# Kernel optimization log

Measured on AMD Instinct MI355X. Metric: run time of the kernel, lower is better.

## Reference

```python
import jax, jax.numpy as jnp
import numpy as np

WS = 8
NUM_HEADS = 4
DIM = 64
H = W = 128
B = 16
EPS = 1e-5


def _rel_pos_index(ws):
    coords = np.stack(np.meshgrid(np.arange(ws), np.arange(ws), indexing='ij'))  # (2,ws,ws)
    cf = coords.reshape(2, -1)
    rel = (cf[:, :, None] - cf[:, None, :]).transpose(1, 2, 0).astype(np.int64)
    rel[..., 0] += ws - 1
    rel[..., 1] += ws - 1
    rel[..., 0] *= 2 * ws - 1
    return jnp.asarray(rel.sum(-1))  # (ws*ws, ws*ws)

_RPI = _rel_pos_index(WS)


def _ln_hw(x, g, b):
    # LayerNorm over last two dims (H,W) of (B,C,H,W), affine shape (H,W)
    mu = x.mean(axis=(-2, -1), keepdims=True)
    var = ((x - mu) ** 2).mean(axis=(-2, -1), keepdims=True)
    return (x - mu) / jnp.sqrt(var + EPS) * g + b


def _ln_c(x, g, b):
    mu = x.mean(-1, keepdims=True)
    var = ((x - mu) ** 2).mean(-1, keepdims=True)
    return (x - mu) / jnp.sqrt(var + EPS) * g + b


def _win_part(x, ws):
    # (B,C,H,W) -> (B*nW, ws*ws, C)
    b, c, hh, ww = x.shape
    x = x.reshape(b, c, hh // ws, ws, ww // ws, ws)
    return x.transpose(0, 2, 4, 3, 5, 1).reshape(b * (hh // ws) * (ww // ws), ws * ws, c)


def _win_rev(w, ws, hh, ww, b):
    # (B*nW, ws*ws, C) -> (B,C,H,W)
    c = w.shape[-1]
    w = w.reshape(b, hh // ws, ww // ws, ws, ws, c)
    return w.transpose(0, 5, 1, 3, 2, 4).reshape(b, c, hh, ww)


def _forward(x, lclg1_ln1_g, lclg1_ln1_b, lclg1_conv_w, lclg1_conv_b, lclg1_ln2_g, lclg1_ln2_b,
             lclg2_ln1_g, lclg2_ln1_b, lclg2_conv_w, lclg2_conv_b, lclg2_ln2_g, lclg2_ln2_b,
             pos1, pos2, q_w, q_b, kv_w, kv_b, rpb_table, gamma, proj_w, proj_b,
             norm2_g, norm2_b, fc1_w, fc1_b, fc2_w, fc2_b):
    b, c, hh, ww = x.shape
    h = NUM_HEADS
    hd = c // h
    n = WS * WS
    scale = hd ** -0.5

    def lclg(z, g1, b1, cw, cb, g2, b2):
        z = _ln_hw(z, g1, b1)
        z = jnp.einsum('oc,bchw->bohw', cw, z) + cb[None, :, None, None]  # 1x1 conv
        return jax.nn.gelu(_ln_hw(z, g2, b2), approximate=False)

    x1 = lclg(x, lclg1_ln1_g, lclg1_ln1_b, lclg1_conv_w, lclg1_conv_b, lclg1_ln2_g, lclg1_ln2_b)
    x2 = lclg(x, lclg2_ln1_g, lclg2_ln1_b, lclg2_conv_w, lclg2_conv_b, lclg2_ln2_g, lclg2_ln2_b)

    x1w = _win_part(x1, WS) + pos1  # (B_, N, C)
    x2w = _win_part(x2, WS) + pos2
    bw = x1w.shape[0]

    q = (x1w @ q_w.T + q_b).reshape(bw, n, h, hd).transpose(0, 2, 1, 3) * scale  # (B_,h,N,hd)
    kv = (x2w @ kv_w.T + kv_b).reshape(bw, n, 2, h, hd).transpose(2, 0, 3, 1, 4)
    k, v = kv[0], kv[1]

    attn = jnp.einsum('bhnd,bhmd->bhnm', q, k)
    bias = rpb_table[_RPI.reshape(-1)].reshape(n, n, h).transpose(2, 0, 1)  # (h,N,N)
    attn = jax.nn.softmax(attn + bias[None], axis=-1)
    o = jnp.einsum('bhnm,bhmd->bhnd', attn, v)  # (B_,h,N,hd)

    # LAM_Module: attention over head_dim channels of (B_,h,N,hd)
    y = o.transpose(0, 3, 1, 2).reshape(bw, hd, h * n)  # (B_,hd,h*N)
    energy = jnp.einsum('bik,bjk->bij', y, y)  # (B_,hd,hd)
    lam = jnp.einsum('bij,bjk->bik', jax.nn.softmax(energy, axis=-1), y)
    y = (gamma * lam + y).reshape(bw, hd, h, n).transpose(0, 2, 3, 1)  # (B_,h,N,hd)

    xo = y.transpose(0, 2, 1, 3).reshape(bw, n, c) + q.transpose(0, 2, 1, 3).reshape(bw, n, c) + x1w
    xo = xo @ proj_w.T + proj_b

    xo = _win_rev(xo, WS, hh, ww, b)  # (B,C,H,W)

    # MLP with pre-norm residual over channel dim
    t = xo.reshape(b, c, hh * ww).transpose(0, 2, 1)  # (B,HW,C)
    tn = _ln_c(t, norm2_g, norm2_b)
    t = t + (jax.nn.gelu(tn @ fc1_w.T + fc1_b, approximate=False) @ fc2_w.T + fc2_b)
    return t.transpose(0, 2, 1).reshape(b, c, hh, ww)


def setup_inputs() -> dict:
    key = jax.random.key(0)
    ks = jax.random.split(key, 16)
    d = DIM

    def rn(i, shape, sc=0.02):
        return jax.random.normal(ks[i], shape, jnp.float32) * sc

    return dict(
        x=jax.random.normal(ks[0], (B, d, H, W), jnp.float32),
        lclg1_ln1_g=jnp.ones((H, W), jnp.float32), lclg1_ln1_b=jnp.zeros((H, W), jnp.float32),
        lclg1_conv_w=rn(1, (d, d)), lclg1_conv_b=jnp.zeros((d,), jnp.float32),
        lclg1_ln2_g=jnp.ones((H, W), jnp.float32), lclg1_ln2_b=jnp.zeros((H, W), jnp.float32),
        lclg2_ln1_g=jnp.ones((H, W), jnp.float32), lclg2_ln1_b=jnp.zeros((H, W), jnp.float32),
        lclg2_conv_w=rn(2, (d, d)), lclg2_conv_b=jnp.zeros((d,), jnp.float32),
        lclg2_ln2_g=jnp.ones((H, W), jnp.float32), lclg2_ln2_b=jnp.zeros((H, W), jnp.float32),
        pos1=jnp.ones((1, WS * WS, d), jnp.float32),
        pos2=jnp.ones((1, WS * WS, d), jnp.float32),
        q_w=rn(3, (d, d)), q_b=jnp.zeros((d,), jnp.float32),
        kv_w=rn(4, (2 * d, d)), kv_b=jnp.zeros((2 * d,), jnp.float32),
        rpb_table=rn(5, ((2 * WS - 1) ** 2, NUM_HEADS)),
        gamma=jnp.full((1,), 0.1, jnp.float32),
        proj_w=rn(6, (d, d)), proj_b=jnp.zeros((d,), jnp.float32),
        norm2_g=jnp.ones((d,), jnp.float32), norm2_b=jnp.zeros((d,), jnp.float32),
        fc1_w=rn(7, (d, d)), fc1_b=jnp.zeros((d,), jnp.float32),
        fc2_w=rn(8, (d, d)), fc2_b=jnp.zeros((d,), jnp.float32),
    )


def reference(x, lclg1_ln1_g, lclg1_ln1_b, lclg1_conv_w, lclg1_conv_b, lclg1_ln2_g, lclg1_ln2_b,
              lclg2_ln1_g, lclg2_ln1_b, lclg2_conv_w, lclg2_conv_b, lclg2_ln2_g, lclg2_ln2_b,
              pos1, pos2, q_w, q_b, kv_w, kv_b, rpb_table, gamma, proj_w, proj_b,
              norm2_g, norm2_b, fc1_w, fc1_b, fc2_w, fc2_b):
    return _forward(x, lclg1_ln1_g, lclg1_ln1_b, lclg1_conv_w, lclg1_conv_b, lclg1_ln2_g, lclg1_ln2_b,
                    lclg2_ln1_g, lclg2_ln1_b, lclg2_conv_w, lclg2_conv_b, lclg2_ln2_g, lclg2_ln2_b,
                    pos1, pos2, q_w, q_b, kv_w, kv_b, rpb_table, gamma, proj_w, proj_b,
                    norm2_g, norm2_b, fc1_w, fc1_b, fc2_w, fc2_b)
```

## Files before the change

### kernel.cpp

```cpp
#include <hip/hip_runtime.h>
#include <hip/hip_bf16.h>

typedef __hip_bfloat16 bf16;
typedef __attribute__((ext_vector_type(8))) short short8;
typedef __attribute__((ext_vector_type(4))) short short4v;
typedef __attribute__((ext_vector_type(4))) float float4v;
typedef __attribute__((ext_vector_type(2))) float float2v;

__device__ __forceinline__ short f2bs(float f){
    union { bf16 h; short s; } u; u.h = __float2bfloat16(f); return u.s;
}
__device__ __forceinline__ float bs2f(short s){
    return __uint_as_float(((unsigned)(unsigned short)s) << 16);
}
__device__ __forceinline__ float gelu_exact(float x){
    return 0.5f * x * (1.0f + erff(x * 0.70710678118654752440f));
}
#define MFMA(a,b,c) __builtin_amdgcn_mfma_f32_16x16x32_bf16((a),(b),(c),0,0,0)

#define HW 16384
#define NPLANE 1048576
#define EPS 1e-5f
#define LS 72

#define OFF_W1   0
#define OFF_W2   4096
#define OFF_QW   8192
#define OFF_KVW  12288
#define OFF_PW   20480
#define OFF_FW1  24576
#define OFF_FW2  28672

__global__ __launch_bounds__(256) void k_pre(const float* __restrict__ x,
                                             float* __restrict__ mu,
                                             float* __restrict__ rinv,
                                             const float* __restrict__ w1, const float* __restrict__ w2,
                                             const float* __restrict__ qw, const float* __restrict__ kvw,
                                             const float* __restrict__ pw, const float* __restrict__ fw1,
                                             const float* __restrict__ fw2,
                                             short* __restrict__ wb, float* __restrict__ rowsum){
    int bi = blockIdx.x;
    int tid = threadIdx.x;
    if (bi < 1024){
        const float* p = x + (size_t)bi * HW;
        float s = 0.f, ss = 0.f;
        for (int i = tid; i < HW/4; i += 256){
            float4v v = *(const float4v*)(p + i*4);
            #pragma unroll
            for (int k = 0; k < 4; k++){ s += v[k]; ss += v[k]*v[k]; }
        }
        __shared__ float rs[256], rss[256];
        rs[tid] = s; rss[tid] = ss; __syncthreads();
        for (int st = 128; st > 0; st >>= 1){
            if (tid < st){ rs[tid] += rs[tid+st]; rss[tid] += rss[tid+st]; }
            __syncthreads();
        }
        if (tid == 0){
            float m = rs[0] * (1.f/HW);
            float v = rss[0] * (1.f/HW) - m*m;
            mu[bi] = m; rinv[bi] = rsqrtf(v + EPS);
        }
    } else if (bi < 1032){
        int wi = bi - 1024;
        const float* src = wi==0?w1: wi==1?w2: wi==2?qw: wi==3?kvw: wi==4?(kvw+4096): wi==5?pw: wi==6?fw1: fw2;
        short* dst = wb + wi*4096;
        int base = tid*16;
        short8 o8[2];
        #pragma unroll
        for (int k = 0; k < 2; k++){
            float4v v0 = *(const float4v*)(src + base + 8*k);
            float4v v1 = *(const float4v*)(src + base + 8*k + 4);
            #pragma unroll
            for (int j = 0; j < 4; j++){ o8[k][j] = f2bs(v0[j]); o8[k][4+j] = f2bs(v1[j]); }
        }
        *(short8*)&dst[base]     = o8[0];
        *(short8*)&dst[base + 8] = o8[1];
    } else {
        if (tid < 128){
            int br = tid >> 6, o = tid & 63;
            const float* W = br ? w2 : w1;
            float s = 0.f;
            for (int c = 0; c < 64; c++) s += W[o*64 + c];
            rowsum[br*64 + o] = s;
        }
    }
}

__global__ __launch_bounds__(256) void k_conv(const float* __restrict__ x,
                                              const float* __restrict__ mu,
                                              const float* __restrict__ rinv,
                                              const float* __restrict__ g1a, const float* __restrict__ b1a,
                                              const float* __restrict__ cb1,
                                              const float* __restrict__ g1b, const float* __restrict__ b1b,
                                              const float* __restrict__ cb2,
                                              const short* __restrict__ wb,
                                              const float* __restrict__ rowsum,
                                              float* __restrict__ partS, float* __restrict__ partQ){
    int blk = blockIdx.x;
    int b = blk >> 8; int tile = blk & 255; int hw0 = tile * 64;
    __shared__ __align__(16) short xn_bf[64*LS];
    const int tid = threadIdx.x;
    const int wq = tid >> 6, lane = tid & 63, qd = lane >> 4, col = lane & 15;
    const float4v zf = {0.f,0.f,0.f,0.f};

    {
        int p = tid & 63, cq = tid >> 6;
        const float* xb = x + (size_t)(b*64 + 16*cq)*HW + hw0 + p;
        float4v m4[4], r4[4];
        #pragma unroll
        for (int k = 0; k < 4; k++){
            m4[k] = *(const float4v*)(mu   + b*64 + 16*cq + 4*k);
            r4[k] = *(const float4v*)(rinv + b*64 + 16*cq + 4*k);
        }
        short8 o8[2];
        #pragma unroll
        for (int k = 0; k < 2; k++)
            #pragma unroll
            for (int j = 0; j < 8; j++){
                int jj = 8*k + j;
                float v = xb[(size_t)jj*HW];
                o8[k][j] = f2bs((v - m4[jj>>2][jj&3]) * r4[jj>>2][jj&3]);
            }
        *(short8*)&xn_bf[p*LS + 16*cq]     = o8[0];
        *(short8*)&xn_bf[p*LS + 16*cq + 8] = o8[1];
    }
    __syncthreads();

    #pragma unroll
    for (int br = 0; br < 2; br++){
        const short* W  = wb + (br ? OFF_W2 : OFF_W1);
        const float* cb = br ? cb2 : cb1;
        const float* gp = br ? g1b : g1a;
        const float* bp = br ? b1b : b1a;
        short8 a0 = *(const short8*)&W[(16*wq + col)*64 + 8*qd];
        short8 a1 = *(const short8*)&W[(16*wq + col)*64 + 32 + 8*qd];
        float cbv[4], rsv[4];
        #pragma unroll
        for (int r = 0; r < 4; r++){
            int o = 16*wq + 4*qd + r;
            cbv[r] = cb[o]; rsv[r] = rowsum[br*64 + o];
        }
        float sa[4]  = {0.f,0.f,0.f,0.f};
        float ssa[4] = {0.f,0.f,0.f,0.f};
        #pragma unroll
        for (int jn = 0; jn < 4; jn++){
            short8 bx0 = *(const short8*)&xn_bf[(16*jn + col)*LS + 8*qd];
            short8 bx1 = *(const short8*)&xn_bf[(16*jn + col)*LS + 32 + 8*qd];
            float4v acc = zf;
            acc = MFMA(a0, bx0, acc);
            acc = MFMA(a1, bx1, acc);
            int hw = hw0 + 16*jn + col;
            float gl = gp[hw], bl = bp[hw];
            #pragma unroll
            for (int r = 0; r < 4; r++){
                float v = gl*acc[r] + bl*rsv[r] + cbv[r];
                sa[r]  += v;
                ssa[r] += v*v;
            }
        }
        #pragma unroll
        for (int r = 0; r < 4; r++){
            float s = sa[r], ss = ssa[r];
            s += __shfl_xor(s, 1); ss += __shfl_xor(ss, 1);
            s += __shfl_xor(s, 2); ss += __shfl_xor(ss, 2);
            s += __shfl_xor(s, 4); ss += __shfl_xor(ss, 4);
            s += __shfl_xor(s, 8); ss += __shfl_xor(ss, 8);
            if (col == 0){
                int o = 16*wq + 4*qd + r;
                size_t pi = ((size_t)(br*16 + b)*64 + o)*256 + tile;
                partS[pi] = s; partQ[pi] = ss;
            }
        }
    }
}

__global__ __launch_bounds__(256) void k_fin(const float* __restrict__ partS,
                                             const float* __restrict__ partQ,
                                             float* __restrict__ mu2,
                                             float* __restrict__ rinv2){
    int row = blockIdx.x*4 + (threadIdx.x >> 6);
    int lane = threadIdx.x & 63;
    float4v a = *(const float4v*)(partS + (size_t)row*256 + lane*4);
    float4v b = *(const float4v*)(partQ + (size_t)row*256 + lane*4);
    float s  = a[0]+a[1]+a[2]+a[3];
    float ss = b[0]+b[1]+b[2]+b[3];
    #pragma unroll
    for (int st = 1; st < 64; st <<= 1){
        s  += __shfl_xor(s,  st);
        ss += __shfl_xor(ss, st);
    }
    if (lane == 0){
        float m = s * (1.f/HW);
        float v = ss * (1.f/HW) - m*m;
        mu2[row] = m; rinv2[row] = rsqrtf(v + EPS);
    }
}

__global__ __launch_bounds__(256, 4) void k_attn(const float* __restrict__ x, float* __restrict__ outp,
                                              const float* __restrict__ mu1, const float* __restrict__ rinv1,
                                              const float* __restrict__ rowsum,
                                              const float* __restrict__ cb1, const float* __restrict__ cb2,
                                              const float* __restrict__ g1a, const float* __restrict__ b1a,
                                              const float* __restrict__ g1b, const float* __restrict__ b1b,
                                              const float* __restrict__ mu2, const float* __restrict__ rinv2,
                                              const float* __restrict__ g2a, const float* __restrict__ b2a,
                                              const float* __restrict__ g2b, const float* __restrict__ b2b,
                                              const float* __restrict__ pos1, const float* __restrict__ pos2,
                                              const short* __restrict__ wb,
                                              const float* __restrict__ qb, const float* __restrict__ kvb,
                                              const float* __restrict__ rpb, const float* __restrict__ gammap,
                                              const float* __restrict__ pb,
                                              const float* __restrict__ n2g, const float* __restrict__ n2b,
                                              const float* __restrict__ fb1,
                                              const float* __restrict__ fb2){
    int B = blockIdx.x;
    int hy = (B & 7) | ((B >> 5) & 8);
    int wx = (((B >> 9) & 7) << 1) | ((B >> 3) & 1);
    int b  = (B >> 4) & 15;

    const short* qwb  = wb + OFF_QW;
    const short* kvwb = wb + OFF_KVW;
    const short* pwb  = wb + OFF_PW;
    const short* f1b  = wb + OFF_FW1;
    const short* f2b  = wb + OFF_FW2;

    __shared__ __align__(16) char smem[40464];
    short* bufA = (short*)smem;
    short* bufK = (short*)(smem + 9216);
    short* bufV = (short*)(smem + 18432);
    short* bufQ = (short*)(smem + 27648);
    float* rpb_lds = (float*)(smem + 36864);
    float* energyS = (float*)(smem + 36864);
    short* soft_bf = (short*)(smem + 37888);
    float* XOf  = (float*)(smem + 18432);
    short* tnb  = (short*)smem;
    short* h1b  = (short*)(smem + 9216);
    float* sumS = (float*)(smem + 36864);
    float* sqS  = (float*)(smem + 37888);
    float* muS  = (float*)(smem + 38912);
    float* rinvS= (float*)(smem + 39168);

    const int tid = threadIdx.x;
    const int wq = tid >> 6, lane = tid & 63, qd = lane >> 4, col = lane & 15;
    size_t base = (size_t)b * NPLANE;
    #define HWOF(t) ((hy*8 + ((t)>>3))*128 + wx*8 + ((t)&7))

    const float4v zf = {0.f,0.f,0.f,0.f};
    const short8 zero8 = {0,0,0,0,0,0,0,0};

    for (int i = tid; i < 900; i += 256) rpb_lds[i] = rpb[i];

    {
        int t = tid & 63, cq = tid >> 6;
        int hw = HWOF(t);
        const float* mup = mu1   + b*64 + 16*cq;
        const float* rvp = rinv1 + b*64 + 16*cq;
        float4v m4[4], r4[4];
        #pragma unroll
        for (int k = 0; k < 4; k++){
            m4[k] = *(const float4v*)(mup + 4*k);
            r4[k] = *(const float4v*)(rvp + 4*k);
        }
        short8 o8[2];
        #pragma unroll
        for (int k = 0; k < 2; k++)
            #pragma unroll
            for (int j = 0; j < 8; j++){
                int jj = 8*k + j;
                float v = x[base + (size_t)(16*cq + jj)*HW + hw];
                o8[k][j] = f2bs((v - m4[jj>>2][jj&3]) * r4[jj>>2][jj&3]);
            }
        *(short8*)&bufV[t*LS + 16*cq]     = o8[0];
        *(short8*)&bufV[t*LS + 16*cq + 8] = o8[1];
    }
    __syncthreads();

    {
        short8 a10 = *(const short8*)&wb[OFF_W1 + (16*wq + col)*64 + 8*qd];
        short8 a11 = *(const short8*)&wb[OFF_W1 + (16*wq + col)*64 + 32 + 8*qd];
        short8 a20 = *(const short8*)&wb[OFF_W2 + (16*wq + col)*64 + 8*qd];
        short8 a21 = *(const short8*)&wb[OFF_W2 + (16*wq + col)*64 + 32 + 8*qd];
        float cb1v[4], rs1v[4], m2a[4], rv2a[4];
        float cb2v[4], rs2v[4], m2b[4], rv2b[4];
        #pragma unroll
        for (int r = 0; r < 4; r++){
            int o = 16*wq + 4*qd + r;
            cb1v[r] = cb1[o]; rs1v[r] = rowsum[o];
            m2a[r] = mu2[b*64 + o]; rv2a[r] = rinv2[b*64 + o];
            cb2v[r] = cb2[o]; rs2v[r] = rowsum[64 + o];
            m2b[r] = mu2[1024 + b*64 + o]; rv2b[r] = rinv2[1024 + b*64 + o];
        }
        #pragma unroll
        for (int jn = 0; jn < 4; jn++){
            int t = 16*jn + col; int hw = HWOF(t);
            short8 bx0 = *(const short8*)&bufV[t*LS + 8*qd];
            short8 bx1 = *(const short8*)&bufV[t*LS + 32 + 8*qd];
            {
                float4v acc = zf;
                acc = MFMA(a10, bx0, acc);
                acc = MFMA(a11, bx1, acc);
                float gl = g1a[hw], bl = b1a[hw], gg = g2a[hw], bo = b2a[hw];
                float4v p4 = *(const float4v*)(pos1 + t*64 + 16*wq + 4*qd);
                short4v pk;
                #pragma unroll
                for (int r = 0; r < 4; r++){
                    float v = gl*acc[r] + bl*rs1v[r] + cb1v[r];
                    float z = (v - m2a[r]) * rv2a[r] * gg + bo;
                    pk[r] = f2bs(gelu_exact(z) + p4[r]);
                }
                *(short4v*)&bufA[t*LS + 16*wq + 4*qd] = pk;
            }
            {
                float4v acc = zf;
                acc = MFMA(a20, bx0, acc);
                acc = MFMA(a21, bx1, acc);
                float gl = g1b[hw], bl = b1b[hw], gg = g2b[hw], bo = b2b[hw];
                float4v p4 = *(const float4v*)(pos2 + t*64 + 16*wq + 4*qd);
                short4v pk;
                #pragma unroll
                for (int r = 0; r < 4; r++){
                    float v = gl*acc[r] + bl*rs2v[r] + cb2v[r];
                    float z = (v - m2b[r]) * rv2b[r] * gg + bo;
                    pk[r] = f2bs(gelu_exact(z) + p4[r]);
                }
                *(short4v*)&bufQ[t*LS + 16*wq + 4*qd] = pk;
            }
        }
    }
    __syncthreads();

    {
        short8 ax0 = *(const short8*)&bufQ[(16*wq + col)*LS + 8*qd];
        short8 ax1 = *(const short8*)&bufQ[(16*wq + col)*LS + 32 + 8*qd];
        #pragma unroll
        for (int jn = 0; jn < 4; jn++){
            int c = 16*jn + col;
            short8 wv0 = *(const short8*)&kvwb[(64 + c)*64 + 8*qd];
            short8 wv1 = *(const short8*)&kvwb[(64 + c)*64 + 32 + 8*qd];
            float4v acc = zf;
            acc = MFMA(ax0, wv0, acc);
            acc = MFMA(ax1, wv1, acc);
            float bv = kvb[64 + c];
            short4v pk;
            #pragma unroll
            for (int r = 0; r < 4; r++) pk[r] = f2bs(acc[r] + bv);
            *(short4v*)&bufV[c*LS + 16*wq + 4*qd] = pk;
        }
        short8 a0 = *(const short8*)&kvwb[(16*wq + col)*64 + 8*qd];
        short8 a1 = *(const short8*)&kvwb[(16*wq + col)*64 + 32 + 8*qd];
        float kbr[4];
        #pragma unroll
        for (int r = 0; r < 4; r++) kbr[r] = kvb[16*wq + 4*qd + r];
        #pragma unroll
        for (int jn = 0; jn < 4; jn++){
            int t = 16*jn + col;
            short8 bx0 = *(const short8*)&bufQ[t*LS + 8*qd];
            short8 bx1 = *(const short8*)&bufQ[t*LS + 32 + 8*qd];
            float4v acc = zf;
            acc = MFMA(a0, bx0, acc);
            acc = MFMA(a1, bx1, acc);
            short4v pk;
            #pragma unroll
            for (int r = 0; r < 4; r++) pk[r] = f2bs(acc[r] + kbr[r]);
            *(short4v*)&bufK[t*LS + 16*wq + 4*qd] = pk;
        }
    }
    __syncthreads();

    {
        short8 a0 = *(const short8*)&qwb[(16*wq + col)*64 + 8*qd];
        short8 a1 = *(const short8*)&qwb[(16*wq + col)*64 + 32 + 8*qd];
        float qbr[4];
        #pragma unroll
        for (int r = 0; r < 4; r++) qbr[r] = qb[16*wq + 4*qd + r];
        #pragma unroll
        for (int jn = 0; jn < 4; jn++){
            int t = 16*jn + col;
            short8 bx0 = *(const short8*)&bufA[t*LS + 8*qd];
            short8 bx1 = *(const short8*)&bufA[t*LS + 32 + 8*qd];
            float4v acc = zf;
            acc = MFMA(a0, bx0, acc);
            acc = MFMA(a1, bx1, acc);
            short4v pk;
            #pragma unroll
            for (int r = 0; r < 4; r++) pk[r] = f2bs((acc[r] + qbr[r]) * 0.25f);
            *(short4v*)&bufQ[t*LS + 16*wq + 4*qd] = pk;
        }
    }
    short4v xreg[4];
    #pragma unroll
    for (int h = 0; h < 4; h++){
        short4v xr;
        #pragma unroll
        for (int r = 0; r < 4; r++)
            xr[r] = bufA[(16*wq + 4*qd + r)*LS + 16*h + col];
        xreg[h] = xr;
    }
    __syncthreads();

    int idx_t[4][4];
    {
        int t = 16*wq + col, ty = t >> 3, tx = t & 7;
        #pragma unroll
        for (int jn = 0; jn < 4; jn++)
            #pragma unroll
            for (int r = 0; r < 4; r++){
                int u = 16*jn + 4*qd + r;
                idx_t[jn][r] = (ty - (u>>3) + 7)*15 + (tx - (u&7) + 7);
            }
    }

    for (int h = 0; h < 4; h++){
        short8 bq = *(const short8*)&bufQ[(16*wq + col)*LS + h*16 + (qd & 1)*8];
        float pr[4][4];
        #pragma unroll
        for (int jn = 0; jn < 4; jn++){
            short8 ak = *(const short8*)&bufK[(16*jn + col)*LS + h*16 + (qd & 1)*8];
            if (qd >= 2) ak = zero8;
            float4v acc = MFMA(ak, bq, zf);
            #pragma unroll
            for (int r = 0; r < 4; r++)
                pr[jn][r] = acc[r] + rpb_lds[idx_t[jn][r]*4 + h];
        }
        float m = pr[0][0];
        #pragma unroll
        for (int jn = 0; jn < 4; jn++)
            #pragma unroll
            for (int r = 0; r < 4; r++) m = fmaxf(m, pr[jn][r]);
        m = fmaxf(m, __shfl_xor(m, 16));
        m = fmaxf(m, __shfl_xor(m, 32));
        float s = 0.f;
        #pragma unroll
        for (int jn = 0; jn < 4; jn++)
            #pragma unroll
            for (int r = 0; r < 4; r++){ pr[jn][r] = __expf(pr[jn][r] - m); s += pr[jn][r]; }
        s += __shfl_xor(s, 16);
        s += __shfl_xor(s, 32);
        float rc = 1.f / s;
        #pragma unroll
        for (int jn = 0; jn < 4; jn++){
            short4v pk;
            #pragma unroll
            for (int r = 0; r < 4; r++) pk[r] = f2bs(pr[jn][r] * rc);
            *(short4v*)&bufA[(16*wq + col)*LS + 16*jn + 4*qd] = pk;
        }
        short8 ap0 = *(const short8*)&bufA[(16*wq + col)*LS + 8*qd];
        short8 ap1 = *(const short8*)&bufA[(16*wq + col)*LS + 32 + 8*qd];
        short8 bv0 = *(const short8*)&bufV[(h*16 + col)*LS + 8*qd];
        short8 bv1 = *(const short8*)&bufV[(h*16 + col)*LS + 32 + 8*qd];
        float4v acc_o = zf;
        acc_o = MFMA(ap0, bv0, acc_o);
        acc_o = MFMA(ap1, bv1, acc_o);
        __syncthreads();
        short4v ot;
        #pragma unroll
        for (int r = 0; r < 4; r++) ot[r] = f2bs(acc_o[r]);
        *(short4v*)&bufV[(h*16 + col)*LS + 16*wq + 4*qd] = ot;
        #pragma unroll
        for (int r = 0; r < 4; r++)
            bufK[(16*wq + 4*qd + r)*LS + h*16 + col] = ot[r];
    }
    __syncthreads();

    {
        float4v acc_e = zf;
        #pragma unroll
        for (int h = 0; h < 4; h++){
            short8 f0 = *(const short8*)&bufV[(h*16 + col)*LS + 8*qd];
            short8 f1 = *(const short8*)&bufV[(h*16 + col)*LS + 32 + 8*qd];
            acc_e = MFMA(f0, f0, acc_e);
            acc_e = MFMA(f1, f1, acc_e);
        }
        if (wq == 0){
            #pragma unroll
            for (int r = 0; r < 4; r++) energyS[(4*qd + r)*16 + col] = acc_e[r];
        }
    }
    __syncthreads();
    if (tid < 16){
        int i = tid; float m = -1e30f;
        for (int j = 0; j < 16; j++) m = fmaxf(m, energyS[i*16 + j]);
        float s = 0.f; float e[16];
        for (int j = 0; j < 16; j++){ e[j] = __expf(energyS[i*16 + j] - m); s += e[j]; }
        float rc = 1.f / s;
        for (int j = 0; j < 16; j++) soft_bf[i*32 + j] = f2bs(e[j] * rc);
        for (int j = 0; j < 16; j++) soft_bf[i*32 + 16 + j] = 0;
    }
    __syncthreads();

    {
        float gam = gammap[0];
        short8 asf = *(const short8*)&soft_bf[col*32 + 8*qd];
        #pragma unroll
        for (int h = 0; h < 4; h++){
            short8 ay = *(const short8*)&bufK[(16*wq + col)*LS + 16*h + (qd & 1)*8];
            float4v acc = MFMA(ay, asf, zf);
            short4v xv = xreg[h];
            #pragma unroll
            for (int r = 0; r < 4; r++){
                int ro = (16*wq + 4*qd + r)*LS + 16*h + col;
                float ot = bs2f(bufK[ro]);
                float qv = bs2f(bufQ[ro]);
                float xo = gam*acc[r] + ot + qv + bs2f(xv[r]);
                bufK[ro] = f2bs(xo);
            }
        }
    }
    __syncthreads();

    {
        short8 a0 = *(const short8*)&pwb[(16*wq + col)*64 + 8*qd];
        short8 a1 = *(const short8*)&pwb[(16*wq + col)*64 + 32 + 8*qd];
        float pbr[4];
        #pragma unroll
        for (int r = 0; r < 4; r++) pbr[r] = pb[16*wq + 4*qd + r];
        #pragma unroll
        for (int jn = 0; jn < 4; jn++){
            int t = 16*jn + col;
            short8 bx0 = *(const short8*)&bufK[t*LS + 8*qd];
            short8 bx1 = *(const short8*)&bufK[t*LS + 32 + 8*qd];
            float4v acc = zf;
            acc = MFMA(a0, bx0, acc);
            acc = MFMA(a1, bx1, acc);
            float2v w0 = {acc[0]+pbr[0], acc[1]+pbr[1]};
            float2v w1 = {acc[2]+pbr[2], acc[3]+pbr[3]};
            *(float2v*)&XOf[t*66 + 16*wq + 4*qd]     = w0;
            *(float2v*)&XOf[t*66 + 16*wq + 4*qd + 2] = w1;
        }
    }
    __syncthreads();

    {
        int p = tid & 63, qg = tid >> 6;
        float s = 0.f, ss = 0.f;
        #pragma unroll
        for (int j = 0; j < 8; j++){
            float2v v = *(const float2v*)&XOf[p*66 + qg*16 + 2*j];
            s += v[0]+v[1]; ss += v[0]*v[0] + v[1]*v[1];
        }
        sumS[qg*64 + p] = s; sqS[qg*64 + p] = ss;
    }
    __syncthreads();
    if (tid < 64){
        float s  = sumS[tid] + sumS[64+tid] + sumS[128+tid] + sumS[192+tid];
        float ss = sqS[tid]  + sqS[64+tid]  + sqS[128+tid]  + sqS[192+tid];
        float m = s * (1.f/64.f);
        float var = ss * (1.f/64.f) - m*m;
        muS[tid] = m; rinvS[tid] = rsqrtf(var + EPS);
    }
    __syncthreads();
    {
        int p = tid & 63, qg = tid >> 6;
        float m = muS[p], rv = rinvS[p];
        short8 o8[2];
        #pragma unroll
        for (int k = 0; k < 2; k++)
            #pragma unroll
            for (int j = 0; j < 8; j++){
                int c = qg*16 + k*8 + j;
                o8[k][j] = f2bs((XOf[p*66 + c] - m) * rv * n2g[c] + n2b[c]);
            }
        *(short8*)&tnb[p*LS + qg*16]     = o8[0];
        *(short8*)&tnb[p*LS + qg*16 + 8] = o8[1];
    }
    __syncthreads();
    {
        short8 a0 = *(const short8*)&f1b[(16*wq + col)*64 + 8*qd];
        short8 a1 = *(const short8*)&f1b[(16*wq + col)*64 + 32 + 8*qd];
        float fbr[4];
        #pragma unroll
        for (int r = 0; r < 4; r++) fbr[r] = fb1[16*wq + 4*qd + r];
        #pragma unroll
        for (int jn = 0; jn < 4; jn++){
            int t = 16*jn + col;
            short8 bx0 = *(const short8*)&tnb[t*LS + 8*qd];
            short8 bx1 = *(const short8*)&tnb[t*LS + 32 + 8*qd];
            float4v acc = zf;
            acc = MFMA(a0, bx0, acc);
            acc = MFMA(a1, bx1, acc);
            short4v pk;
            #pragma unroll
            for (int r = 0; r < 4; r++) pk[r] = f2bs(gelu_exact(acc[r] + fbr[r]));
            *(short4v*)&h1b[t*LS + 16*wq + 4*qd] = pk;
        }
    }
    __syncthreads();
    {
        short8 a0 = *(const short8*)&h1b[(16*wq + col)*LS + 8*qd];
        short8 a1 = *(const short8*)&h1b[(16*wq + col)*LS + 32 + 8*qd];
        #pragma unroll
        for (int jn = 0; jn < 4; jn++){
            int c2 = 16*jn + col;
            short8 f0 = *(const short8*)&f2b[c2*64 + 8*qd];
            short8 f1 = *(const short8*)&f2b[c2*64 + 32 + 8*qd];
            float4v acc = zf;
            acc = MFMA(a0, f0, acc);
            acc = MFMA(a1, f1, acc);
            float bv = fb2[c2];
            float4v ov;
            #pragma unroll
            for (int r = 0; r < 4; r++)
                ov[r] = acc[r] + bv + XOf[(16*wq + 4*qd + r)*66 + c2];
            int t0 = 16*wq + 4*qd;
            *(float4v*)(outp + base + (size_t)c2*HW + HWOF(t0)) = ov;
        }
    }
    #undef HWOF
}

extern "C" void kernel_launch(void* const* d_in, const int* in_sizes, int n_in,
                              void* d_out, int out_size, void* d_ws, size_t ws_size,
                              hipStream_t stream){
    const float* x        = (const float*)d_in[0];
    const float* l1_g1    = (const float*)d_in[1];
    const float* l1_b1    = (const float*)d_in[2];
    const float* l1_cw    = (const float*)d_in[3];
    const float* l1_cb    = (const float*)d_in[4];
    const float* l1_g2    = (const float*)d_in[5];
    const float* l1_b2    = (const float*)d_in[6];
    const float* l2_g1    = (const float*)d_in[7];
    const float* l2_b1    = (const float*)d_in[8];
    const float* l2_cw    = (const float*)d_in[9];
    const float* l2_cb    = (const float*)d_in[10];
    const float* l2_g2    = (const float*)d_in[11];
    const float* l2_b2    = (const float*)d_in[12];
    const float* pos1     = (const float*)d_in[13];
    const float* pos2     = (const float*)d_in[14];
    const float* q_w      = (const float*)d_in[15];
    const float* q_b      = (const float*)d_in[16];
    const float* kv_w     = (const float*)d_in[17];
    const float* kv_b     = (const float*)d_in[18];
    const float* rpb      = (const float*)d_in[19];
    const float* gamma    = (const float*)d_in[20];
    const float* proj_w   = (const float*)d_in[21];
    const float* proj_b   = (const float*)d_in[22];
    const float* norm2_g  = (const float*)d_in[23];
    const float* norm2_b  = (const float*)d_in[24];
    const float* fc1_w    = (const float*)d_in[25];
    const float* fc1_b    = (const float*)d_in[26];
    const float* fc2_w    = (const float*)d_in[27];
    const float* fc2_b    = (const float*)d_in[28];

    float* out = (float*)d_out;

    float* partS = (float*)d_ws;
    float* partQ = partS + (size_t)2048*256;
    float* mu1   = partQ + (size_t)2048*256;
    float* rinv1 = mu1 + 1024;
    float* mu2   = rinv1 + 1024;
    float* rinv2 = mu2 + 2048;
    float* rowsumG = rinv2 + 2048;
    short* wbuf  = (short*)(rowsumG + 128);

    k_pre  <<<1033, 256, 0, stream>>>(x, mu1, rinv1,
                                      l1_cw, l2_cw, q_w, kv_w, proj_w, fc1_w, fc2_w,
                                      wbuf, rowsumG);
    k_conv <<<4096, 256, 0, stream>>>(x, mu1, rinv1,
                                      l1_g1, l1_b1, l1_cb,
                                      l2_g1, l2_b1, l2_cb,
                                      wbuf, rowsumG,
                                      partS, partQ);
    k_fin  <<<512, 256, 0, stream>>>(partS, partQ, mu2, rinv2);
    k_attn <<<4096, 256, 0, stream>>>(x, out, mu1, rinv1, rowsumG,
                                      l1_cb, l2_cb,
                                      l1_g1, l1_b1, l2_g1, l2_b1,
                                      mu2, rinv2,
                                      l1_g2, l1_b2, l2_g2, l2_b2,
                                      pos1, pos2, wbuf, q_b, kv_b,
                                      rpb, gamma, proj_b,
                                      norm2_g, norm2_b, fc1_b, fc2_b);
}
```

Before: 322.9 us.

## Give conv-stat blocks four tiles each, hoist weights, and approximate erf in GELU

k_conv now has each block loop over four 64-pixel tiles, with weights, biases and row sums loaded once into registers, and both branches computed per tile. This cuts the grid from 4096 to 1024 blocks and shrinks the partial-sum buffers, so k_fin reduces 64 partials per row instead of 256. GELU swaps erff for an Abramowitz-Stegun polynomial using a fast reciprocal and __expf. That polynomial has error around 1e-7 and may shift accuracy slightly. The fewer, longer blocks also add per-tile barriers and may hide latency less well.

Result: faster. 316.5 us (-2.0%).

```diff
diff --git a/kernel.cpp b/kernel.cpp
--- a/kernel.cpp
+++ b/kernel.cpp
@@ -14,7 +14,14 @@
     return __uint_as_float(((unsigned)(unsigned short)s) << 16);
 }
 __device__ __forceinline__ float gelu_exact(float x){
-    return 0.5f * x * (1.0f + erff(x * 0.70710678118654752440f));
+    float ax = fabsf(x) * 0.70710678118654752440f;
+    float t  = __builtin_amdgcn_rcpf(fmaf(0.3275911f, ax, 1.0f));
+    float poly = t*fmaf(t, fmaf(t, fmaf(t, fmaf(t, 1.061405429f, -1.453152027f),
+                                 1.421413741f), -0.284496736f), 0.254829592f);
+    float e = __expf(-ax*ax);
+    float erfp = fmaf(-poly, e, 1.0f);
+    float er = copysignf(erfp, x);
+    return 0.5f * x * (1.0f + er);
 }
 #define MFMA(a,b,c) __builtin_amdgcn_mfma_f32_16x16x32_bf16((a),(b),(c),0,0,0)
 
@@ -86,7 +93,7 @@
     }
 }
 
-__global__ __launch_bounds__(256) void k_conv(const float* __restrict__ x,
+__global__ __launch_bounds__(256, 4) void k_conv(const float* __restrict__ x,
                                               const float* __restrict__ mu,
                                               const float* __restrict__ rinv,
                                               const float* __restrict__ g1a, const float* __restrict__ b1a,
@@ -97,81 +104,96 @@
                                               const float* __restrict__ rowsum,
                                               float* __restrict__ partS, float* __restrict__ partQ){
     int blk = blockIdx.x;
-    int b = blk >> 8; int tile = blk & 255; int hw0 = tile * 64;
+    int b = blk >> 6; int chunk = blk & 63;
     __shared__ __align__(16) short xn_bf[64*LS];
     const int tid = threadIdx.x;
     const int wq = tid >> 6, lane = tid & 63, qd = lane >> 4, col = lane & 15;
     const float4v zf = {0.f,0.f,0.f,0.f};
-
-    {
-        int p = tid & 63, cq = tid >> 6;
-        const float* xb = x + (size_t)(b*64 + 16*cq)*HW + hw0 + p;
-        float4v m4[4], r4[4];
-        #pragma unroll
-        for (int k = 0; k < 4; k++){
-            m4[k] = *(const float4v*)(mu   + b*64 + 16*cq + 4*k);
-            r4[k] = *(const float4v*)(rinv + b*64 + 16*cq + 4*k);
-        }
-        short8 o8[2];
-        #pragma unroll
-        for (int k = 0; k < 2; k++)
-            #pragma unroll
-            for (int j = 0; j < 8; j++){
-                int jj = 8*k + j;
-                float v = xb[(size_t)jj*HW];
-                o8[k][j] = f2bs((v - m4[jj>>2][jj&3]) * r4[jj>>2][jj&3]);
-            }
-        *(short8*)&xn_bf[p*LS + 16*cq]     = o8[0];
-        *(short8*)&xn_bf[p*LS + 16*cq + 8] = o8[1];
-    }
-    __syncthreads();
-
+    const int p = tid & 63, cq = tid >> 6;
+
+    float4v m4[4], r4[4];
     #pragma unroll
-    for (int br = 0; br < 2; br++){
-        const short* W  = wb + (br ? OFF_W2 : OFF_W1);
-        const float* cb = br ? cb2 : cb1;
-        const float* gp = br ? g1b : g1a;
-        const float* bp = br ? b1b : b1a;
-        short8 a0 = *(const short8*)&W[(16*wq + col)*64 + 8*qd];
-        short8 a1 = *(const short8*)&W[(16*wq + col)*64 + 32 + 8*qd];
-        float cbv[4], rsv[4];
-        #pragma unroll
-        for (int r = 0; r < 4; r++){
-            int o = 16*wq + 4*qd + r;
-            cbv[r] = cb[o]; rsv[r] = rowsum[br*64 + o];
-        }
-        float sa[4]  = {0.f,0.f,0.f,0.f};
-        float ssa[4] = {0.f,0.f,0.f,0.f};
+    for (int k = 0; k < 4; k++){
+        m4[k] = *(const float4v*)(mu   + b*64 + 16*cq + 4*k);
+        r4[k] = *(const float4v*)(rinv + b*64 + 16*cq + 4*k);
+    }
+    short8 a10 = *(const short8*)&wb[OFF_W1 + (16*wq + col)*64 + 8*qd];
+    short8 a11 = *(const short8*)&wb[OFF_W1 + (16*wq + col)*64 + 32 + 8*qd];
+    short8 a20 = *(const short8*)&wb[OFF_W2 + (16*wq + col)*64 + 8*qd];
+    short8 a21 = *(const short8*)&wb[OFF_W2 + (16*wq + col)*64 + 32 + 8*qd];
+    float cb1v[4], rs1v[4], cb2v[4], rs2v[4];
+    #pragma unroll
+    for (int r = 0; r < 4; r++){
+        int o = 16*wq + 4*qd + r;
+        cb1v[r] = cb1[o]; rs1v[r] = rowsum[o];
+        cb2v[r] = cb2[o]; rs2v[r] = rowsum[64 + o];
+    }
+    float sa[2][4]  = {{0.f,0.f,0.f,0.f},{0.f,0.f,0.f,0.f}};
+    float ssa[2][4] = {{0.f,0.f,0.f,0.f},{0.f,0.f,0.f,0.f}};
+
+    for (int tl = 0; tl < 4; tl++){
+        int hw0 = chunk*256 + tl*64;
+        {
+            const float* xb = x + (size_t)(b*64 + 16*cq)*HW + hw0 + p;
+            short8 o8[2];
+            #pragma unroll
+            for (int k = 0; k < 2; k++)
+                #pragma unroll
+                for (int j = 0; j < 8; j++){
+                    int jj = 8*k + j;
+                    float v = xb[(size_t)jj*HW];
+                    o8[k][j] = f2bs((v - m4[jj>>2][jj&3]) * r4[jj>>2][jj&3]);
+                }
+            *(short8*)&xn_bf[p*LS + 16*cq]     = o8[0];
+            *(short8*)&xn_bf[p*LS + 16*cq + 8] = o8[1];
+        }
+        __syncthreads();
         #pragma unroll
         for (int jn = 0; jn < 4; jn++){
             short8 bx0 = *(const short8*)&xn_bf[(16*jn + col)*LS + 8*qd];
             short8 bx1 = *(const short8*)&xn_bf[(16*jn + col)*LS + 32 + 8*qd];
-            float4v acc = zf;
-            acc = MFMA(a0, bx0, acc);
-            acc = MFMA(a1, bx1, acc);
             int hw = hw0 + 16*jn + col;
-            float gl = gp[hw], bl = bp[hw];
-            #pragma unroll
-            for (int r = 0; r < 4; r++){
-                float v = gl*acc[r] + bl*rsv[r] + cbv[r];
-                sa[r]  += v;
-                ssa[r] += v*v;
-            }
-        }
+            {
+                float4v acc = zf;
+                acc = MFMA(a10, bx0, acc);
+                acc = MFMA(a11, bx1, acc);
+                float gl = g1a[hw], bl = b1a[hw];
+                #pragma unroll
+                for (int r = 0; r < 4; r++){
+                    float v = gl*acc[r] + bl*rs1v[r] + cb1v[r];
+                    sa[0][r] += v; ssa[0][r] += v*v;
+                }
+            }
+            {
+                float4v acc = zf;
+                acc = MFMA(a20, bx0, acc);
+                acc = MFMA(a21, bx1, acc);
+                float gl = g1b[hw], bl = b1b[hw];
+                #pragma unroll
+                for (int r = 0; r < 4; r++){
+                    float v = gl*acc[r] + bl*rs2v[r] + cb2v[r];
+                    sa[1][r] += v; ssa[1][r] += v*v;
+                }
+            }
+        }
+        __syncthreads();
+    }
+
+    #pragma unroll
+    for (int br = 0; br < 2; br++)
         #pragma unroll
         for (int r = 0; r < 4; r++){
-            float s = sa[r], ss = ssa[r];
+            float s = sa[br][r], ss = ssa[br][r];
             s += __shfl_xor(s, 1); ss += __shfl_xor(ss, 1);
             s += __shfl_xor(s, 2); ss += __shfl_xor(ss, 2);
             s += __shfl_xor(s, 4); ss += __shfl_xor(ss, 4);
             s += __shfl_xor(s, 8); ss += __shfl_xor(ss, 8);
             if (col == 0){
                 int o = 16*wq + 4*qd + r;
-                size_t pi = ((size_t)(br*16 + b)*64 + o)*256 + tile;
+                size_t pi = ((size_t)(br*16 + b)*64 + o)*64 + chunk;
                 partS[pi] = s; partQ[pi] = ss;
             }
         }
-    }
 }
 
 __global__ __launch_bounds__(256) void k_fin(const float* __restrict__ partS,
@@ -180,10 +202,8 @@
                                              float* __restrict__ rinv2){
     int row = blockIdx.x*4 + (threadIdx.x >> 6);
     int lane = threadIdx.x & 63;
-    float4v a = *(const float4v*)(partS + (size_t)row*256 + lane*4);
-    float4v b = *(const float4v*)(partQ + (size_t)row*256 + lane*4);
-    float s  = a[0]+a[1]+a[2]+a[3];
-    float ss = b[0]+b[1]+b[2]+b[3];
+    float s  = partS[(size_t)row*64 + lane];
+    float ss = partQ[(size_t)row*64 + lane];
     #pragma unroll
     for (int st = 1; st < 64; st <<= 1){
         s  += __shfl_xor(s,  st);
@@ -644,8 +664,8 @@
     float* out = (float*)d_out;
 
     float* partS = (float*)d_ws;
-    float* partQ = partS + (size_t)2048*256;
-    float* mu1   = partQ + (size_t)2048*256;
+    float* partQ = partS + (size_t)2048*64;
+    float* mu1   = partQ + (size_t)2048*64;
     float* rinv1 = mu1 + 1024;
     float* mu2   = rinv1 + 1024;
     float* rinv2 = mu2 + 2048;
@@ -655,7 +675,7 @@
     k_pre  <<<1033, 256, 0, stream>>>(x, mu1, rinv1,
                                       l1_cw, l2_cw, q_w, kv_w, proj_w, fc1_w, fc2_w,
                                       wbuf, rowsumG);
-    k_conv <<<4096, 256, 0, stream>>>(x, mu1, rinv1,
+    k_conv <<<1024, 256, 0, stream>>>(x, mu1, rinv1,
                                       l1_g1, l1_b1, l1_cb,
                                       l2_g1, l2_b1, l2_cb,
                                       wbuf, rowsumG,
```
